# Kernel tuning notes

Measured on AMD Instinct MI355X. Metric: run time of the kernel, lower is better.

## Reference

```python
import jax, jax.numpy as jnp
import numpy as np

N_NODES = 100000
N_EDGES = 3200000
D_IN = 256
D_OUT = 256


def setup_inputs() -> dict:
    key = jax.random.key(0)
    k1, k2, k3, k4, k5 = jax.random.split(key, 5)
    x = jax.random.normal(k1, (N_NODES, D_IN), dtype=jnp.float32)
    weight = jax.random.normal(k2, (D_IN, D_OUT), dtype=jnp.float32) * (1.0 / np.sqrt(D_IN))
    edge_row = jax.random.randint(k3, (N_EDGES,), 0, N_NODES, dtype=jnp.int32)
    edge_col = jax.random.randint(k4, (N_EDGES,), 0, N_NODES, dtype=jnp.int32)
    edge_val = jax.random.uniform(k5, (N_EDGES,), dtype=jnp.float32)
    return {"x": x, "weight": weight, "edge_row": edge_row,
            "edge_col": edge_col, "edge_val": edge_val}


def reference(x, weight, edge_row, edge_col, edge_val):
    # support = dropout(x) @ W  (dropout p=0 -> identity, eval-mode math)
    support = x @ weight                       # [N, D_OUT]
    # output = spmm(adj, support): for each edge (r, c, v): out[r] += v * support[c]
    gathered = edge_val[:, None] * support[edge_col]   # [E, D_OUT]
    output = jax.ops.segment_sum(gathered, edge_row, num_segments=N_NODES)
    return output
```

## Files before the change

kernel.cpp:

```cpp
#include <hip/hip_runtime.h>

#define N_NODES 100000
#define N_EDGES 3200000
#define DIM 256

typedef _Float16 half_t;
typedef __attribute__((ext_vector_type(4))) _Float16 half4;
typedef __attribute__((ext_vector_type(8))) _Float16 half8;
typedef __attribute__((ext_vector_type(4))) float floatx4;

__global__ __launch_bounds__(256) void castw_kernel(const float* __restrict__ w,
                                                    half_t* __restrict__ wT) {
    __shared__ float tile[32][33];
    int bk = blockIdx.x * 32;
    int bn = blockIdx.y * 32;
    int tx = threadIdx.x & 31, ty = threadIdx.x >> 5;
#pragma unroll
    for (int i = 0; i < 4; i++)
        tile[ty + i * 8][tx] = w[(size_t)(bk + ty + i * 8) * DIM + bn + tx];
    __syncthreads();
#pragma unroll
    for (int i = 0; i < 4; i++)
        wT[(size_t)(bn + ty + i * 8) * DIM + bk + tx] = (half_t)tile[tx][ty + i * 8];
}

#define BM 128
#define BN 128
#define BK 32
#define LDK 40

__global__ __launch_bounds__(256) void gemm_f16_kernel(const float* __restrict__ A,
                                                       const half_t* __restrict__ BT,
                                                       half_t* __restrict__ C, int M) {
    __shared__ half_t As[BM][LDK];
    __shared__ half_t Bs[BN][LDK];

    const int tid = threadIdx.x;
    const int wid = tid >> 6, lane = tid & 63;
    const int wm = wid & 1, wn = wid >> 1;
    const int row0 = blockIdx.x * BM;
    const int col0 = blockIdx.y * BN;
    const int lr = lane & 15;
    const int quad = lane >> 4;

    floatx4 acc[4][4] = {};

    const int ar = tid >> 1;
    const int ac = (tid & 1) * 16;
    const bool avalid = (row0 + ar) < M;
    const float* aptr = A + (size_t)(row0 + ar) * DIM + ac;

    for (int k0 = 0; k0 < DIM; k0 += BK) {
        {
            const float4* src = (const float4*)(aptr + k0);
            half_t* dst = &As[ar][ac];
#pragma unroll
            for (int i = 0; i < 4; i++) {
                float4 v = avalid ? src[i] : make_float4(0.f, 0.f, 0.f, 0.f);
                half4 h;
                h.x = (half_t)v.x; h.y = (half_t)v.y;
                h.z = (half_t)v.z; h.w = (half_t)v.w;
                ((half4*)dst)[i] = h;
            }
        }
        {
#pragma unroll
            for (int i = 0; i < 2; i++) {
                int ch = tid + i * 256;
                int r = ch >> 2, cb = (ch & 3) * 8;
                half8 v = *(const half8*)(BT + (size_t)(col0 + r) * DIM + k0 + cb);
                *(half8*)&Bs[r][cb] = v;
            }
        }
        __syncthreads();

        half8 a[4], b[4];
#pragma unroll
        for (int i = 0; i < 4; i++)
            a[i] = *(const half8*)&As[wm * 64 + i * 16 + lr][quad * 8];
#pragma unroll
        for (int j = 0; j < 4; j++)
            b[j] = *(const half8*)&Bs[wn * 64 + j * 16 + lr][quad * 8];
#pragma unroll
        for (int i = 0; i < 4; i++)
#pragma unroll
            for (int j = 0; j < 4; j++)
                acc[i][j] = __builtin_amdgcn_mfma_f32_16x16x32_f16(a[i], b[j], acc[i][j], 0, 0, 0);
        __syncthreads();
    }

#pragma unroll
    for (int i = 0; i < 4; i++) {
#pragma unroll
        for (int j = 0; j < 4; j++) {
            int gc = col0 + wn * 64 + j * 16 + lr;
            int grb = row0 + wm * 64 + i * 16 + quad * 4;
#pragma unroll
            for (int r = 0; r < 4; r++) {
                int gr = grb + r;
                if (gr < M) C[(size_t)gr * DIM + gc] = (half_t)acc[i][j][r];
            }
        }
    }
}

#define NBUCK 391
#define EPB 4096
#define NEB ((N_EDGES + EPB - 1) / EPB)

__global__ __launch_bounds__(256) void bucket_hist_kernel(const int* __restrict__ erow,
                                                          int* __restrict__ bcnt) {
    __shared__ int lh[NBUCK];
    for (int b = threadIdx.x; b < NBUCK; b += 256) lh[b] = 0;
    __syncthreads();
    int base4 = blockIdx.x * (EPB / 4);
#pragma unroll
    for (int i = 0; i < 4; i++) {
        int idx4 = base4 + i * 256 + threadIdx.x;
        if (idx4 < N_EDGES / 4) {
            int4 r4 = ((const int4*)erow)[idx4];
            atomicAdd(&lh[r4.x >> 8], 1);
            atomicAdd(&lh[r4.y >> 8], 1);
            atomicAdd(&lh[r4.z >> 8], 1);
            atomicAdd(&lh[r4.w >> 8], 1);
        }
    }
    __syncthreads();
    for (int b = threadIdx.x; b < NBUCK; b += 256)
        if (lh[b]) atomicAdd(&bcnt[b * 16], lh[b]);
}

__global__ __launch_bounds__(512) void scan_buckets_kernel(int* __restrict__ bcnt,
                                                           int* __restrict__ bbase,
                                                           int* __restrict__ offsets) {
    __shared__ int s[512];
    int t = threadIdx.x;
    int v = (t < NBUCK) ? bcnt[t * 16] : 0;
    s[t] = v;
    __syncthreads();
    for (int off = 1; off < 512; off <<= 1) {
        int u = (t >= off) ? s[t - off] : 0;
        __syncthreads();
        s[t] += u;
        __syncthreads();
    }
    if (t < NBUCK) {
        int ex = s[t] - v;
        bbase[t] = ex;
        bcnt[t * 16] = ex;
    }
    if (t == 0) { bbase[NBUCK] = N_EDGES; offsets[N_NODES] = N_EDGES; }
}

__global__ __launch_bounds__(256) void bucket_scatter_kernel(const int* __restrict__ erow,
                                                             const int* __restrict__ ecol,
                                                             const float* __restrict__ eval,
                                                             int* __restrict__ bcursor,
                                                             int2* __restrict__ tmp) {
    __shared__ int lh[NBUCK];
    __shared__ int lbase[NBUCK];
    for (int b = threadIdx.x; b < NBUCK; b += 256) lh[b] = 0;
    __syncthreads();

    int base4 = blockIdx.x * (EPB / 4);
    int4 r4[4], c4[4];
    float4 v4[4];
    bool ok[4];
#pragma unroll
    for (int i = 0; i < 4; i++) {
        int idx4 = base4 + i * 256 + threadIdx.x;
        ok[i] = idx4 < N_EDGES / 4;
        if (ok[i]) {
            r4[i] = ((const int4*)erow)[idx4];
            c4[i] = ((const int4*)ecol)[idx4];
            v4[i] = ((const float4*)eval)[idx4];
            atomicAdd(&lh[r4[i].x >> 8], 1);
            atomicAdd(&lh[r4[i].y >> 8], 1);
            atomicAdd(&lh[r4[i].z >> 8], 1);
            atomicAdd(&lh[r4[i].w >> 8], 1);
        }
    }
    __syncthreads();
    for (int b = threadIdx.x; b < NBUCK; b += 256) {
        int c = lh[b];
        lbase[b] = c ? atomicAdd(&bcursor[b * 16], c) : 0;
        lh[b] = 0;
    }
    __syncthreads();

#define SCAT(R, C, V)                                                     \
    {                                                                     \
        int _r = (R), _c = (C);                                           \
        int _b = _r >> 8;                                                 \
        int _rank = atomicAdd(&lh[_b], 1);                                \
        tmp[lbase[_b] + _rank] =                                          \
            make_int2(((_r & 255) << 17) | _c, __float_as_int(V));        \
    }
#pragma unroll
    for (int i = 0; i < 4; i++) {
        if (!ok[i]) continue;
        SCAT(r4[i].x, c4[i].x, v4[i].x);
        SCAT(r4[i].y, c4[i].y, v4[i].y);
        SCAT(r4[i].z, c4[i].z, v4[i].z);
        SCAT(r4[i].w, c4[i].w, v4[i].w);
    }
#undef SCAT
}

__global__ __launch_bounds__(256) void bucket_to_csr_kernel(const int2* __restrict__ tmp,
                                                            const int* __restrict__ bbase,
                                                            int* __restrict__ offsets,
                                                            int2* __restrict__ sedge) {
    __shared__ int lh[256];
    __shared__ int s[256];
    const int b = blockIdx.x;
    const int t = threadIdx.x;
    const int beg = bbase[b], end = bbase[b + 1];

    lh[t] = 0;
    __syncthreads();
    for (int e = beg + t; e < end; e += 256)
        atomicAdd(&lh[tmp[e].x >> 17], 1);
    __syncthreads();

    int c = lh[t];
    s[t] = c;
    __syncthreads();
    for (int off = 1; off < 256; off <<= 1) {
        int u = (t >= off) ? s[t - off] : 0;
        __syncthreads();
        s[t] += u;
        __syncthreads();
    }
    int ex = s[t] - c;
    int row = (b << 8) + t;
    if (row < N_NODES) offsets[row] = beg + ex;
    lh[t] = ex;
    __syncthreads();

    for (int e = beg + t; e < end; e += 256) {
        int2 q = tmp[e];
        int lr = q.x >> 17;
        int rank = atomicAdd(&lh[lr], 1);
        sedge[beg + rank] = make_int2(q.x & 0x1FFFF, q.y);
    }
}

__global__ __launch_bounds__(256) void spmm_kernel(const half_t* __restrict__ support,
                                                   const int* __restrict__ offsets,
                                                   const int2* __restrict__ edges,
                                                   float* __restrict__ out) {
    int row = (blockIdx.x * blockDim.x + threadIdx.x) >> 6;
    if (row >= N_NODES) return;
    int lane = threadIdx.x & 63;
    int h = lane >> 5;
    int j = lane & 31;

    int beg = offsets[row];
    int end = offsets[row + 1];

    float acc[8] = {0.f, 0.f, 0.f, 0.f, 0.f, 0.f, 0.f, 0.f};
    int e = beg;
    for (; e + 7 < end; e += 8) {
        int2 q0 = edges[e + h];
        int2 q1 = edges[e + 2 + h];
        int2 q2 = edges[e + 4 + h];
        int2 q3 = edges[e + 6 + h];
        half8 s0 = *(const half8*)(support + (size_t)q0.x * DIM + j * 8);
        half8 s1 = *(const half8*)(support + (size_t)q1.x * DIM + j * 8);
        half8 s2 = *(const half8*)(support + (size_t)q2.x * DIM + j * 8);
        half8 s3 = *(const half8*)(support + (size_t)q3.x * DIM + j * 8);
        float v0 = __int_as_float(q0.y), v1 = __int_as_float(q1.y);
        float v2 = __int_as_float(q2.y), v3 = __int_as_float(q3.y);
#pragma unroll
        for (int d = 0; d < 8; d++)
            acc[d] += v0 * (float)s0[d] + v1 * (float)s1[d]
                    + v2 * (float)s2[d] + v3 * (float)s3[d];
    }
    for (; e + 1 < end; e += 2) {
        int2 q0 = edges[e + h];
        half8 s0 = *(const half8*)(support + (size_t)q0.x * DIM + j * 8);
        float v0 = __int_as_float(q0.y);
#pragma unroll
        for (int d = 0; d < 8; d++) acc[d] += v0 * (float)s0[d];
    }
    if (e < end) {
        int2 q0 = edges[e];
        half8 s0 = *(const half8*)(support + (size_t)q0.x * DIM + j * 8);
        float v0 = (h == 0) ? __int_as_float(q0.y) : 0.f;
#pragma unroll
        for (int d = 0; d < 8; d++) acc[d] += v0 * (float)s0[d];
    }

    float r0, r1, r2, r3, g0, g1, g2, g3;
    if (h == 0) {
        r0 = acc[0]; r1 = acc[1]; r2 = acc[2]; r3 = acc[3];
        g0 = acc[4]; g1 = acc[5]; g2 = acc[6]; g3 = acc[7];
    } else {
        r0 = acc[4]; r1 = acc[5]; r2 = acc[6]; r3 = acc[7];
        g0 = acc[0]; g1 = acc[1]; g2 = acc[2]; g3 = acc[3];
    }
    r0 += __shfl_xor(g0, 32, 64);
    r1 += __shfl_xor(g1, 32, 64);
    r2 += __shfl_xor(g2, 32, 64);
    r3 += __shfl_xor(g3, 32, 64);

    *(float4*)(out + (size_t)row * DIM + j * 8 + h * 4) = make_float4(r0, r1, r2, r3);
}

extern "C" void kernel_launch(void* const* d_in, const int* in_sizes, int n_in,
                              void* d_out, int out_size, void* d_ws, size_t ws_size,
                              hipStream_t stream) {
    const float* x    = (const float*)d_in[0];
    const float* w    = (const float*)d_in[1];
    const int*   erow = (const int*)d_in[2];
    const int*   ecol = (const int*)d_in[3];
    const float* eval = (const float*)d_in[4];
    float* out = (float*)d_out;

    char* ws = (char*)d_ws;
    half_t* support = (half_t*)ws;
    int*    offsets = (int*)(ws + 51200000);
    int2*   sedge   = (int2*)(ws + 51600128);
    half_t* wT      = (half_t*)(ws + 77200128);
    int*    bcnt    = (int*)(ws + 77331200);
    int*    bbase   = (int*)(ws + 77356224);
    int2*   tmp     = (int2*)d_out;

    hipMemsetAsync(bcnt, 0, NBUCK * 16 * sizeof(int), stream);

    castw_kernel<<<dim3(8, 8), 256, 0, stream>>>(w, wT);

    dim3 ggrid((N_NODES + BM - 1) / BM, DIM / BN);
    gemm_f16_kernel<<<ggrid, 256, 0, stream>>>(x, wT, support, N_NODES);

    bucket_hist_kernel<<<NEB, 256, 0, stream>>>(erow, bcnt);
    scan_buckets_kernel<<<1, 512, 0, stream>>>(bcnt, bbase, offsets);
    bucket_scatter_kernel<<<NEB, 256, 0, stream>>>(erow, ecol, eval, bcnt, tmp);
    bucket_to_csr_kernel<<<NBUCK, 256, 0, stream>>>(tmp, bbase, offsets, sedge);

    spmm_kernel<<<(N_NODES * 64 + 255) / 256, 256, 0, stream>>>(support, offsets,
                                                                sedge, out);
}
```

Measured before the change: 566.0 us.

## Widen GEMM tile to full N, enlarge bucket blocks, unroll SpMM with vector edge loads

```diff
diff --git a/kernel.cpp b/kernel.cpp
--- a/kernel.cpp
+++ b/kernel.cpp
@@ -25,28 +25,26 @@
 }
 
 #define BM 128
-#define BN 128
 #define BK 32
 #define LDK 40
 
-__global__ __launch_bounds__(256) void gemm_f16_kernel(const float* __restrict__ A,
+__global__ __launch_bounds__(512) void gemm_f16_kernel(const float* __restrict__ A,
                                                        const half_t* __restrict__ BT,
                                                        half_t* __restrict__ C, int M) {
     __shared__ half_t As[BM][LDK];
-    __shared__ half_t Bs[BN][LDK];
+    __shared__ half_t Bs[256][LDK];
 
     const int tid = threadIdx.x;
     const int wid = tid >> 6, lane = tid & 63;
     const int wm = wid & 1, wn = wid >> 1;
     const int row0 = blockIdx.x * BM;
-    const int col0 = blockIdx.y * BN;
     const int lr = lane & 15;
     const int quad = lane >> 4;
 
     floatx4 acc[4][4] = {};
 
-    const int ar = tid >> 1;
-    const int ac = (tid & 1) * 16;
+    const int ar = tid >> 2;
+    const int ac = (tid & 3) * 8;
     const bool avalid = (row0 + ar) < M;
     const float* aptr = A + (size_t)(row0 + ar) * DIM + ac;
 
@@ -55,7 +53,7 @@
             const float4* src = (const float4*)(aptr + k0);
             half_t* dst = &As[ar][ac];
 #pragma unroll
-            for (int i = 0; i < 4; i++) {
+            for (int i = 0; i < 2; i++) {
                 float4 v = avalid ? src[i] : make_float4(0.f, 0.f, 0.f, 0.f);
                 half4 h;
                 h.x = (half_t)v.x; h.y = (half_t)v.y;
@@ -66,9 +64,9 @@
         {
 #pragma unroll
             for (int i = 0; i < 2; i++) {
-                int ch = tid + i * 256;
+                int ch = tid + i * 512;
                 int r = ch >> 2, cb = (ch & 3) * 8;
-                half8 v = *(const half8*)(BT + (size_t)(col0 + r) * DIM + k0 + cb);
+                half8 v = *(const half8*)(BT + (size_t)r * DIM + k0 + cb);
                 *(half8*)&Bs[r][cb] = v;
             }
         }
@@ -93,7 +91,7 @@
     for (int i = 0; i < 4; i++) {
 #pragma unroll
         for (int j = 0; j < 4; j++) {
-            int gc = col0 + wn * 64 + j * 16 + lr;
+            int gc = wn * 64 + j * 16 + lr;
             int grb = row0 + wm * 64 + i * 16 + quad * 4;
 #pragma unroll
             for (int r = 0; r < 4; r++) {
@@ -105,7 +103,7 @@
 }
 
 #define NBUCK 391
-#define EPB 4096
+#define EPB 16384
 #define NEB ((N_EDGES + EPB - 1) / EPB)
 
 __global__ __launch_bounds__(256) void bucket_hist_kernel(const int* __restrict__ erow,
@@ -115,7 +113,7 @@
     __syncthreads();
     int base4 = blockIdx.x * (EPB / 4);
 #pragma unroll
-    for (int i = 0; i < 4; i++) {
+    for (int i = 0; i < 16; i++) {
         int idx4 = base4 + i * 256 + threadIdx.x;
         if (idx4 < N_EDGES / 4) {
             int4 r4 = ((const int4*)erow)[idx4];
@@ -163,21 +161,15 @@
     __syncthreads();
 
     int base4 = blockIdx.x * (EPB / 4);
-    int4 r4[4], c4[4];
-    float4 v4[4];
-    bool ok[4];
-#pragma unroll
-    for (int i = 0; i < 4; i++) {
+#pragma unroll
+    for (int i = 0; i < 16; i++) {
         int idx4 = base4 + i * 256 + threadIdx.x;
-        ok[i] = idx4 < N_EDGES / 4;
-        if (ok[i]) {
-            r4[i] = ((const int4*)erow)[idx4];
-            c4[i] = ((const int4*)ecol)[idx4];
-            v4[i] = ((const float4*)eval)[idx4];
-            atomicAdd(&lh[r4[i].x >> 8], 1);
-            atomicAdd(&lh[r4[i].y >> 8], 1);
-            atomicAdd(&lh[r4[i].z >> 8], 1);
-            atomicAdd(&lh[r4[i].w >> 8], 1);
+        if (idx4 < N_EDGES / 4) {
+            int4 r4 = ((const int4*)erow)[idx4];
+            atomicAdd(&lh[r4.x >> 8], 1);
+            atomicAdd(&lh[r4.y >> 8], 1);
+            atomicAdd(&lh[r4.z >> 8], 1);
+            atomicAdd(&lh[r4.w >> 8], 1);
         }
     }
     __syncthreads();
@@ -197,12 +189,17 @@
             make_int2(((_r & 255) << 17) | _c, __float_as_int(V));        \
     }
 #pragma unroll
-    for (int i = 0; i < 4; i++) {
-        if (!ok[i]) continue;
-        SCAT(r4[i].x, c4[i].x, v4[i].x);
-        SCAT(r4[i].y, c4[i].y, v4[i].y);
-        SCAT(r4[i].z, c4[i].z, v4[i].z);
-        SCAT(r4[i].w, c4[i].w, v4[i].w);
+    for (int i = 0; i < 16; i++) {
+        int idx4 = base4 + i * 256 + threadIdx.x;
+        if (idx4 < N_EDGES / 4) {
+            int4 r4 = ((const int4*)erow)[idx4];
+            int4 c4 = ((const int4*)ecol)[idx4];
+            float4 v4 = ((const float4*)eval)[idx4];
+            SCAT(r4.x, c4.x, v4.x);
+            SCAT(r4.y, c4.y, v4.y);
+            SCAT(r4.z, c4.z, v4.z);
+            SCAT(r4.w, c4.w, v4.w);
+        }
     }
 #undef SCAT
 }
@@ -261,21 +258,39 @@
 
     float acc[8] = {0.f, 0.f, 0.f, 0.f, 0.f, 0.f, 0.f, 0.f};
     int e = beg;
-    for (; e + 7 < end; e += 8) {
-        int2 q0 = edges[e + h];
-        int2 q1 = edges[e + 2 + h];
-        int2 q2 = edges[e + 4 + h];
-        int2 q3 = edges[e + 6 + h];
+
+    if ((e & 1) && e < end) {
+        int2 q0 = edges[e];
         half8 s0 = *(const half8*)(support + (size_t)q0.x * DIM + j * 8);
-        half8 s1 = *(const half8*)(support + (size_t)q1.x * DIM + j * 8);
-        half8 s2 = *(const half8*)(support + (size_t)q2.x * DIM + j * 8);
-        half8 s3 = *(const half8*)(support + (size_t)q3.x * DIM + j * 8);
-        float v0 = __int_as_float(q0.y), v1 = __int_as_float(q1.y);
-        float v2 = __int_as_float(q2.y), v3 = __int_as_float(q3.y);
+        float v0 = (h == 0) ? __int_as_float(q0.y) : 0.f;
+#pragma unroll
+        for (int d = 0; d < 8; d++) acc[d] += v0 * (float)s0[d];
+        e++;
+    }
+
+    for (; e + 15 < end; e += 16) {
+        int4 pa = *(const int4*)(edges + e + 2 * h);
+        int4 pb = *(const int4*)(edges + e + 4 + 2 * h);
+        int4 pc = *(const int4*)(edges + e + 8 + 2 * h);
+        int4 pd = *(const int4*)(edges + e + 12 + 2 * h);
+        half8 s0 = *(const half8*)(support + (size_t)pa.x * DIM + j * 8);
+        half8 s1 = *(const half8*)(support + (size_t)pa.z * DIM + j * 8);
+        half8 s2 = *(const half8*)(support + (size_t)pb.x * DIM + j * 8);
+        half8 s3 = *(const half8*)(support + (size_t)pb.z * DIM + j * 8);
+        half8 s4 = *(const half8*)(support + (size_t)pc.x * DIM + j * 8);
+        half8 s5 = *(const half8*)(support + (size_t)pc.z * DIM + j * 8);
+        half8 s6 = *(const half8*)(support + (size_t)pd.x * DIM + j * 8);
+        half8 s7 = *(const half8*)(support + (size_t)pd.z * DIM + j * 8);
+        float v0 = __int_as_float(pa.y), v1 = __int_as_float(pa.w);
+        float v2 = __int_as_float(pb.y), v3 = __int_as_float(pb.w);
+        float v4 = __int_as_float(pc.y), v5 = __int_as_float(pc.w);
+        float v6 = __int_as_float(pd.y), v7 = __int_as_float(pd.w);
 #pragma unroll
         for (int d = 0; d < 8; d++)
             acc[d] += v0 * (float)s0[d] + v1 * (float)s1[d]
-                    + v2 * (float)s2[d] + v3 * (float)s3[d];
+                    + v2 * (float)s2[d] + v3 * (float)s3[d]
+                    + v4 * (float)s4[d] + v5 * (float)s5[d]
+                    + v6 * (float)s6[d] + v7 * (float)s7[d];
     }
     for (; e + 1 < end; e += 2) {
         int2 q0 = edges[e + h];
@@ -331,8 +346,8 @@
 
     castw_kernel<<<dim3(8, 8), 256, 0, stream>>>(w, wT);
 
-    dim3 ggrid((N_NODES + BM - 1) / BM, DIM / BN);
-    gemm_f16_kernel<<<ggrid, 256, 0, stream>>>(x, wT, support, N_NODES);
+    dim3 ggrid((N_NODES + BM - 1) / BM, 1);
+    gemm_f16_kernel<<<ggrid, 512, 0, stream>>>(x, wT, support, N_NODES);
 
     bucket_hist_kernel<<<NEB, 256, 0, stream>>>(erow, bcnt);
     scan_buckets_kernel<<<1, 512, 0, stream>>>(bcnt, bbase, offsets);
```

Result: faster. 544.4 us (-3.8%).
